# Performance work log

Measured on AMD Instinct MI355X. Metric: run time of the kernel, lower is better.

Reference implementation:

```python
import jax, jax.numpy as jnp
import numpy as np

N_NODES = 50000
N_EDGES = 500000
D_NODE = 256
D_EDGE = 256
FINAL_OUT = 256
NEG_SLOPE = 0.01  # torch LeakyReLU default


def _linear_params(key, d_in, d_out):
    kw, kb = jax.random.split(key)
    s = 1.0 / np.sqrt(d_in)
    W = jax.random.uniform(kw, (d_in, d_out), jnp.float32, -s, s)
    b = jax.random.uniform(kb, (d_out,), jnp.float32, -s, s)
    return W, b


def setup_inputs() -> dict:
    key = jax.random.key(0)
    ks = jax.random.split(key, 8)
    in1 = D_NODE + D_EDGE          # 512
    hid1 = 2 * in1                 # 1024
    out1 = hid1 // 2               # 512
    in2 = out1 + D_NODE            # 768
    hid2 = 2 * in2                 # 1536
    W1, b1 = _linear_params(ks[0], in1, hid1)
    W2, b2 = _linear_params(ks[1], hid1, out1)
    W3, b3 = _linear_params(ks[2], in2, hid2)
    W4, b4 = _linear_params(ks[3], hid2, FINAL_OUT)
    x = jax.random.normal(ks[4], (N_NODES, D_NODE), jnp.float32)
    edge_attr = jax.random.normal(ks[5], (N_EDGES, D_EDGE), jnp.float32)
    edge_index = jax.random.randint(ks[6], (2, N_EDGES), 0, N_NODES, jnp.int64)
    u = jax.random.normal(ks[7], (1, 16), jnp.float32)
    batch = jnp.zeros((N_NODES,), jnp.int64)
    return {"x": x, "edge_index": edge_index, "edge_attr": edge_attr,
            "u": u, "batch": batch,
            "W1": W1, "b1": b1, "W2": W2, "b2": b2,
            "W3": W3, "b3": b3, "W4": W4, "b4": b4}


def _leaky(v):
    return jnp.where(v >= 0, v, NEG_SLOPE * v)


def reference(x, edge_index, edge_attr, u, batch, W1, b1, W2, b2, W3, b3, W4, b4):
    row, col = edge_index[0], edge_index[1]
    # gather source-node features and concat edge features: [E, D_NODE+D_EDGE]
    m = jnp.concatenate([x[row], edge_attr], axis=1)
    # node_mlp_1
    m = _leaky(m @ W1 + b1) @ W2 + b2            # [E, out1]
    # scatter-mean over destination nodes (count clamped to 1, as torch_scatter)
    agg = jax.ops.segment_sum(m, col, num_segments=x.shape[0])
    cnt = jax.ops.segment_sum(jnp.ones((m.shape[0],), m.dtype), col,
                              num_segments=x.shape[0])
    agg = agg / jnp.maximum(cnt, 1.0)[:, None]   # [N, out1]
    # node_mlp_2
    h = jnp.concatenate([x, agg], axis=1)        # [N, in2]
    return _leaky(h @ W3 + b3) @ W4 + b4         # [N, FINAL_OUT]
```

## Files before the change

kernel.cpp:

```cpp
#include <hip/hip_runtime.h>

typedef __bf16 bf16x8 __attribute__((ext_vector_type(8)));
typedef float fx4 __attribute__((ext_vector_type(4)));
typedef unsigned short u16x8 __attribute__((ext_vector_type(8)));
typedef unsigned short u16x4 __attribute__((ext_vector_type(4)));

__device__ __forceinline__ unsigned short f2b(float f) {
  unsigned u = __float_as_uint(f);
  u = (u + 0x7fffu + ((u >> 16) & 1u)) >> 16;
  return (unsigned short)u;
}
__device__ __forceinline__ float b2f(unsigned short s) {
  return __uint_as_float((unsigned)s << 16);
}

__device__ __forceinline__ void gload16(const void* g, void* l) {
  __builtin_amdgcn_global_load_lds(
      (const __attribute__((address_space(1))) unsigned int*)g,
      (__attribute__((address_space(3))) unsigned int*)l, 16, 0, 0);
}

template<int MODE, int K, int N, int NT, bool EAB>
__global__ __launch_bounds__(256)
void gemm_k(const unsigned short* __restrict__ A,
            const unsigned short* __restrict__ xb,
            const unsigned short* __restrict__ eas,
            const float* __restrict__ eaf,
            const float* __restrict__ aggH_in,
            const float* __restrict__ cnt,
            const unsigned short* __restrict__ agg2b_in,
            const unsigned short* __restrict__ zxb,
            const int* __restrict__ perm,
            const int* __restrict__ ssrc,
            const int* __restrict__ sdst,
            const unsigned short* __restrict__ Bt,
            const float* __restrict__ bias,
            float* __restrict__ outf,
            unsigned short* __restrict__ outb,
            int M, int base, int mt, int mtc)
{
  const int bid = blockIdx.x;
  const int xcd = bid & 7;
  const int sl  = bid >> 3;
  const int tile_n = sl % NT;
  const int tile_m = xcd * mtc + sl / NT;
  if (tile_m >= mt) return;
  const int mbase = tile_m * 128;

  constexpr int SMEM = (MODE == 1) ? 51216 : ((MODE == 2) ? 16384 : 32768);
  __shared__ __align__(16) char smem[SMEM];

  const int t = threadIdx.x;
  const int w = t >> 6, l = t & 63;
  const int wr = w >> 1, wc = w & 1;
  const int lr = l & 15, lk = l >> 4;

  fx4 zero = {0.f, 0.f, 0.f, 0.f};
  fx4 acc[4][4];
#pragma unroll
  for (int i = 0; i < 4; i++)
#pragma unroll
    for (int j = 0; j < 4; j++) acc[i][j] = zero;

  auto STAGE = [&](int ks, int b) {
    const int k0 = ks * 32;
    char* Ab = (char*)smem + b * 16384;
    char* Bb = Ab + 8192;
#pragma unroll
    for (int it = 0; it < 2; ++it) {
      const int c = t + it * 256;
      const int row = c >> 2, u = c & 3;
      gload16(Bt + (size_t)(tile_n * 128 + row) * K + (k0 + u * 8),
              Bb + c * 16);
      int rl = mbase + row; if (rl >= M) rl = M - 1;
      if constexpr (MODE == 1) {
        if constexpr (EAB) {
          gload16(eas + (size_t)rl * 256 + (k0 + u * 8), Ab + c * 16);
        } else {
          const int e = perm[rl];
          const float* s = eaf + (size_t)e * 256 + (k0 + u * 8);
          fx4 f0 = *(const fx4*)s, f1 = *(const fx4*)(s + 4);
          u16x8 v;
          v[0]=f2b(f0[0]); v[1]=f2b(f0[1]); v[2]=f2b(f0[2]); v[3]=f2b(f0[3]);
          v[4]=f2b(f1[0]); v[5]=f2b(f1[1]); v[6]=f2b(f1[2]); v[7]=f2b(f1[3]);
          *(u16x8*)(Ab + c * 16) = v;
        }
      } else if constexpr (MODE == 2) {
        const float ct = cnt[rl];
        const float rs = 1.f / fmaxf(ct, 1.f);
        const float* s = aggH_in + (size_t)rl * 1024 + (k0 + u * 8);
        fx4 f0 = *(const fx4*)s, f1 = *(const fx4*)(s + 4);
        u16x8 v;
        v[0]=f2b(f0[0]*rs); v[1]=f2b(f0[1]*rs); v[2]=f2b(f0[2]*rs); v[3]=f2b(f0[3]*rs);
        v[4]=f2b(f1[0]*rs); v[5]=f2b(f1[1]*rs); v[6]=f2b(f1[2]*rs); v[7]=f2b(f1[3]*rs);
        *(u16x8*)(Ab + c * 16) = v;
      } else if constexpr (MODE == 3) {
        const int node = base + rl;
        if (k0 < 256)
          gload16(xb + (size_t)node * 256 + (k0 + u * 8), Ab + c * 16);
        else
          gload16(agg2b_in + (size_t)node * 512 + (k0 - 256) + u * 8,
                  Ab + c * 16);
      } else if constexpr (MODE == 5) {
        gload16(xb + (size_t)rl * 256 + (k0 + u * 8), Ab + c * 16);
      } else {
        gload16(A + (size_t)rl * K + (k0 + u * 8), Ab + c * 16);
      }
    }
  };

  auto COMPUTE = [&](int b) {
    const unsigned short* Al = (const unsigned short*)((char*)smem + b * 16384);
    const unsigned short* Bl = Al + 4096;
    bf16x8 af[4], bfr[4];
    const int mb0 = wr * 64, nb0 = wc * 64;
#pragma unroll
    for (int i = 0; i < 4; i++)
      af[i] = *(const bf16x8*)(Al + (mb0 + i * 16 + lr) * 32 + lk * 8);
#pragma unroll
    for (int j = 0; j < 4; j++)
      bfr[j] = *(const bf16x8*)(Bl + (nb0 + j * 16 + lr) * 32 + lk * 8);
#pragma unroll
    for (int i = 0; i < 4; i++)
#pragma unroll
      for (int j = 0; j < 4; j++)
        acc[i][j] = __builtin_amdgcn_mfma_f32_16x16x32_bf16(af[i], bfr[j],
                                                            acc[i][j], 0, 0, 0);
  };

  const int NK = K / 32;
  if constexpr (MODE == 1) {
#pragma unroll
    for (int q = 0; q < 8; ++q) {
      const int c = q * 256 + t;
      const int zrow = c >> 4, zu = c & 15;
      int gr = mbase + zrow; if (gr >= M) gr = M - 1;
      gload16(zxb + (size_t)ssrc[gr] * 1024 + tile_n * 128 + zu * 8,
              (char*)smem + 18448 + c * 16);
    }
    for (int ks = 0; ks < NK; ++ks) {
      STAGE(ks, 0);
      __syncthreads();
      COMPUTE(0);
      __syncthreads();
    }
  } else if constexpr (MODE == 2) {
    for (int ks = 0; ks < NK; ++ks) {
      STAGE(ks, 0);
      __syncthreads();
      COMPUTE(0);
      __syncthreads();
    }
  } else {
    STAGE(0, 0);
    for (int ks = 0; ks < NK; ++ks) {
      const int cur = ks & 1;
      if (ks + 1 < NK) {
        STAGE(ks + 1, cur ^ 1);
        asm volatile("s_waitcnt vmcnt(4)" ::: "memory");
      } else {
        asm volatile("s_waitcnt vmcnt(0)" ::: "memory");
      }
      __builtin_amdgcn_s_barrier();
      COMPUTE(cur);
      __builtin_amdgcn_s_barrier();
    }
  }

  if constexpr (MODE == 1) {
    int rows = M - mbase; if (rows > 128) rows = 128;
    unsigned short* CL = (unsigned short*)smem;
    int* runs_s = (int*)(smem + 16896);
    int* runs_e = (int*)(smem + 17408);
    int* runs_d = (int*)(smem + 17920);
    unsigned long long* wmask = (unsigned long long*)(smem + 18432);
    const unsigned short* ZL = (const unsigned short*)(smem + 18448);
    int flag = 0;
    if (t < 128)
      flag = (t < rows) && ((t == 0) || (sdst[mbase + t] != sdst[mbase + t - 1]));
    unsigned long long bm = __ballot(flag);
    if (l == 0 && w < 2) wmask[w] = bm;
    __syncthreads();
    const unsigned long long m0 = wmask[0], m1 = wmask[1];
    const int nruns = __builtin_popcountll(m0) + __builtin_popcountll(m1);
    if (flag) {
      int rank, rend;
      if (t < 64) {
        rank = __builtin_popcountll(m0 & ((t == 0) ? 0ull : ((1ull << t) - 1)));
        unsigned long long above = (t == 63) ? 0ull : (m0 & (~0ull << (t + 1)));
        if (above) rend = __builtin_ctzll(above);
        else if (m1) rend = 64 + __builtin_ctzll(m1);
        else rend = rows;
      } else {
        const int tt = t - 64;
        rank = __builtin_popcountll(m0) +
               __builtin_popcountll(m1 & ((tt == 0) ? 0ull : ((1ull << tt) - 1)));
        unsigned long long above = (tt == 63) ? 0ull : (m1 & (~0ull << (tt + 1)));
        rend = above ? 64 + __builtin_ctzll(above) : rows;
      }
      runs_s[rank] = t; runs_e[rank] = rend; runs_d[rank] = sdst[mbase + t];
    }
    const int lc = wc * 16 + lr;
    const int nn_base = tile_n * 128 + wc * 64 + lr;
    for (int jj = 0; jj < 2; ++jj) {
#pragma unroll
      for (int jp = 0; jp < 2; ++jp) {
        const int j = jj * 2 + jp;
        const float bj = bias[nn_base + j * 16];
        const int cloc = wc * 64 + j * 16 + lr;
#pragma unroll
        for (int i = 0; i < 4; i++)
#pragma unroll
          for (int r = 0; r < 4; r++) {
            const int lrow = wr * 64 + i * 16 + lk * 4 + r;
            float v = acc[i][j][r] + bj + b2f(ZL[lrow * 128 + cloc]);
            v = v >= 0.f ? v : 0.01f * v;
            CL[lrow * 66 + jp * 32 + lc] = f2b(v);
          }
      }
      __syncthreads();
      for (int task = t; task < nruns * 64; task += 256) {
        const int ri = task >> 6, c = task & 63;
        const int rs = runs_s[ri], re = runs_e[ri];
        float s = 0.f;
        for (int r = rs; r < re; ++r) s += b2f(CL[r * 66 + c]);
        const int jp = c >> 5, w16 = (c >> 4) & 1, clr = c & 15;
        const int n = tile_n * 128 + w16 * 64 + (jj * 2 + jp) * 16 + clr;
        float* addr = outf + (size_t)runs_d[ri] * 1024 + n;
        const bool open = (rs == 0 && mbase > 0) || (re == rows && mbase + rows < M);
        if (open) atomicAdd(addr, s); else *addr = s;
      }
      __syncthreads();
    }
  } else {
#pragma unroll
    for (int j = 0; j < 4; j++) {
      const int n = tile_n * 128 + wc * 64 + j * 16 + lr;
      float bj = 0.f;
      if constexpr (MODE == 2 || MODE == 3 || MODE == 4) bj = bias[n];
#pragma unroll
      for (int i = 0; i < 4; i++) {
        const int m0 = mbase + wr * 64 + i * 16 + lk * 4;
#pragma unroll
        for (int r = 0; r < 4; r++) {
          const int m = m0 + r;
          if (m < M) {
            float v = acc[i][j][r];
            if constexpr (MODE == 2) {
              v += (cnt[m] > 0.f ? bj : 0.f);
              outb[(size_t)m * N + n] = f2b(v);
            } else if constexpr (MODE == 3) {
              v += bj;
              v = v >= 0.f ? v : 0.01f * v;
              outb[(size_t)m * N + n] = f2b(v);
            } else if constexpr (MODE == 5) {
              outb[(size_t)m * N + n] = f2b(v);
            } else {
              outf[(size_t)(base + m) * N + n] = v + bj;
            }
          }
        }
      }
    }
  }
}

__global__ void fix_idx_k(const int* __restrict__ src, int* __restrict__ dst, int n2) {
  int i = blockIdx.x * blockDim.x + threadIdx.x;
  if (i >= n2) return;
  bool is64 = true;
#pragma unroll
  for (int p = 0; p < 16; ++p) is64 = is64 && (src[2 * p + 1] == 0);
  dst[i] = is64 ? src[2 * i] : src[i];
}

__global__ void cvt_f2b_k(const float* __restrict__ x, unsigned short* __restrict__ o,
                          long n4) {
  long i = (long)blockIdx.x * blockDim.x + threadIdx.x;
  if (i < n4) {
    fx4 f = *(const fx4*)(x + i * 4);
    u16x4 v; v[0]=f2b(f[0]); v[1]=f2b(f[1]); v[2]=f2b(f[2]); v[3]=f2b(f[3]);
    *(u16x4*)(o + i * 4) = v;
  }
}

__global__ void cvt_eas_k(const float* __restrict__ ea, const int* __restrict__ perm,
                          unsigned short* __restrict__ eas, int E) {
  long i = (long)blockIdx.x * blockDim.x + threadIdx.x;
  if (i >= (long)E * 64) return;
  const int s = (int)(i >> 6), q = (int)(i & 63);
  const float* src = ea + (size_t)perm[s] * 256 + q * 4;
  fx4 f = *(const fx4*)src;
  u16x4 v; v[0]=f2b(f[0]); v[1]=f2b(f[1]); v[2]=f2b(f[2]); v[3]=f2b(f[3]);
  *(u16x4*)(eas + (size_t)s * 256 + q * 4) = v;
}

__global__ void cvt_w_k(const float* __restrict__ W, unsigned short* __restrict__ Wt,
                        int K, int N) {
  long i = (long)blockIdx.x * blockDim.x + threadIdx.x;
  if (i < (long)K * N) {
    int k = (int)(i / N), n = (int)(i % N);
    Wt[(size_t)n * K + k] = f2b(W[i]);
  }
}

__global__ void cnt_kk(const int* __restrict__ ecol, float* __restrict__ cnt, int E) {
  int i = blockIdx.x * blockDim.x + threadIdx.x;
  if (i < E) atomicAdd(cnt + ecol[i], 1.f);
}

__global__ __launch_bounds__(1024)
void scan_k(const float* __restrict__ cnt, int* __restrict__ pos, int Nn) {
  __shared__ int sdata[1024];
  __shared__ int carry;
  if (threadIdx.x == 0) carry = 0;
  __syncthreads();
  for (int bb = 0; bb < Nn; bb += 1024) {
    const int i = bb + threadIdx.x;
    const int v = (i < Nn) ? (int)cnt[i] : 0;
    sdata[threadIdx.x] = v;
    __syncthreads();
    for (int off = 1; off < 1024; off <<= 1) {
      int tv = (threadIdx.x >= off) ? sdata[threadIdx.x - off] : 0;
      __syncthreads();
      sdata[threadIdx.x] += tv;
      __syncthreads();
    }
    const int excl = sdata[threadIdx.x] - v + carry;
    if (i < Nn) pos[i] = excl;
    __syncthreads();
    if (threadIdx.x == 1023) carry += sdata[1023];
    __syncthreads();
  }
}

__global__ void perm_k(const int* __restrict__ idx, int E, int* __restrict__ pos,
                       int* __restrict__ perm, int* __restrict__ ssrc,
                       int* __restrict__ sdst) {
  int e = blockIdx.x * blockDim.x + threadIdx.x;
  if (e >= E) return;
  const int d = idx[E + e];
  const int s = atomicAdd(pos + d, 1);
  perm[s] = e;
  ssrc[s] = idx[e];
  sdst[s] = d;
}

extern "C" void kernel_launch(void* const* d_in, const int* in_sizes, int n_in,
                              void* d_out, int out_size, void* d_ws, size_t ws_size,
                              hipStream_t stream)
{
  const float* x  = (const float*)d_in[0];
  const int* eraw = (const int*)d_in[1];
  const float* ea = (const float*)d_in[2];
  const float* W1 = (const float*)d_in[5];
  const float* b1 = (const float*)d_in[6];
  const float* W2 = (const float*)d_in[7];
  const float* b2 = (const float*)d_in[8];
  const float* W3 = (const float*)d_in[9];
  const float* b3 = (const float*)d_in[10];
  const float* W4 = (const float*)d_in[11];
  const float* b4 = (const float*)d_in[12];
  float* out = (float*)d_out;

  const int Nn = in_sizes[0] / 256;
  const int E  = in_sizes[1] / 2;

  char* p = (char*)d_ws;
  auto take = [&](size_t bytes) -> char* {
    char* r = p; p += (bytes + 255) & ~(size_t)255; return r;
  };
  unsigned short* W1xt = (unsigned short*)take((size_t)1024 * 256 * 2);
  unsigned short* W1et = (unsigned short*)take((size_t)1024 * 256 * 2);
  unsigned short* W2t  = (unsigned short*)take((size_t)1024 * 512 * 2);
  unsigned short* W3t  = (unsigned short*)take((size_t)768 * 1536 * 2);
  unsigned short* W4t  = (unsigned short*)take((size_t)1536 * 256 * 2);
  int* idx  = (int*)take((size_t)2 * E * 4);
  float* cnt  = (float*)take((size_t)Nn * 4);
  float* aggH = (float*)take((size_t)Nn * 1024 * 4);
  size_t zlen = (size_t)(p - (char*)cnt);
  unsigned short* agg2b = (unsigned short*)take((size_t)Nn * 512 * 2);
  unsigned short* xb    = (unsigned short*)take((size_t)Nn * 256 * 2);
  unsigned short* zxb   = (unsigned short*)take((size_t)Nn * 1024 * 2);
  int* pos  = (int*)take((size_t)Nn * 4);
  int* perm = (int*)take((size_t)E * 4);
  int* ssrc = (int*)take((size_t)E * 4);
  int* sdst = (int*)take((size_t)E * 4);

  long avail = (long)ws_size - (long)(p - (char*)d_ws);

  unsigned short* eas = nullptr;
  const long eas_bytes = (((long)E * 256 * 2) + 255) & ~255L;
  if (avail >= eas_bytes + 128 * 3072 + 1024) {
    eas = (unsigned short*)take((size_t)E * 256 * 2);
    avail -= eas_bytes;
  }
  long bandN = avail / 3072;  bandN &= ~127L;
  if (bandN > 50048) bandN = 50048;
  if (bandN < 128)   bandN = 128;
  unsigned short* H3 = (unsigned short*)take((size_t)bandN * 3072);

  hipMemsetAsync(cnt, 0, zlen, stream);
  fix_idx_k<<<(2 * E + 255) / 256, 256, 0, stream>>>(eraw, idx, 2 * E);
  cnt_kk<<<(E + 255) / 256, 256, 0, stream>>>(idx + E, cnt, E);
  scan_k<<<1, 1024, 0, stream>>>(cnt, pos, Nn);
  perm_k<<<(E + 255) / 256, 256, 0, stream>>>(idx, E, pos, perm, ssrc, sdst);
  cvt_f2b_k<<<(Nn * 64 + 255) / 256, 256, 0, stream>>>(x, xb, (long)Nn * 64);
  if (eas)
    cvt_eas_k<<<(int)(((long)E * 64 + 255) / 256), 256, 0, stream>>>(ea, perm,
                                                                     eas, E);
  cvt_w_k<<<(256 * 1024 + 255) / 256, 256, 0, stream>>>(W1, W1xt, 256, 1024);
  cvt_w_k<<<(256 * 1024 + 255) / 256, 256, 0, stream>>>(W1 + 256 * 1024, W1et,
                                                        256, 1024);
  cvt_w_k<<<(1024 * 512 + 255) / 256, 256, 0, stream>>>(W2, W2t, 1024, 512);
  cvt_w_k<<<(768 * 1536 + 255) / 256, 256, 0, stream>>>(W3, W3t, 768, 1536);
  cvt_w_k<<<(1536 * 256 + 255) / 256, 256, 0, stream>>>(W4, W4t, 1536, 256);

  {
    const int mt = (Nn + 127) / 128, mtc = (mt + 7) / 8;
    gemm_k<5, 256, 1024, 8, false><<<mtc * 8 * 8, 256, 0, stream>>>(
        nullptr, xb, nullptr, nullptr, nullptr, nullptr, nullptr, nullptr,
        nullptr, nullptr, nullptr, W1xt, nullptr, nullptr, zxb, Nn, 0, mt, mtc);
  }

  {
    const int mt = (E + 127) / 128, mtc = (mt + 7) / 8;
    const int grid = mtc * 8 * 8;
    if (eas)
      gemm_k<1, 256, 1024, 8, true><<<grid, 256, 0, stream>>>(
          nullptr, nullptr, eas, ea, nullptr, nullptr, nullptr, zxb, perm,
          ssrc, sdst, W1et, b1, aggH, nullptr, E, 0, mt, mtc);
    else
      gemm_k<1, 256, 1024, 8, false><<<grid, 256, 0, stream>>>(
          nullptr, nullptr, nullptr, ea, nullptr, nullptr, nullptr, zxb, perm,
          ssrc, sdst, W1et, b1, aggH, nullptr, E, 0, mt, mtc);
  }

  {
    const int mt = (Nn + 127) / 128, mtc = (mt + 7) / 8;
    gemm_k<2, 1024, 512, 4, false><<<mtc * 8 * 4, 256, 0, stream>>>(
        nullptr, nullptr, nullptr, nullptr, aggH, cnt, nullptr, nullptr,
        nullptr, nullptr, nullptr, W2t, b2, nullptr, agg2b, Nn, 0, mt, mtc);
  }

  for (long base = 0; base < Nn; base += bandN) {
    long rem = Nn - base;
    int mb = (int)(rem < bandN ? rem : bandN);
    int mt = (mb + 127) / 128, mtc = (mt + 7) / 8;
    gemm_k<3, 768, 1536, 12, false><<<mtc * 8 * 12, 256, 0, stream>>>(
        nullptr, xb, nullptr, nullptr, nullptr, nullptr, agg2b, nullptr,
        nullptr, nullptr, nullptr, W3t, b3, nullptr, H3, mb, (int)base, mt, mtc);
    gemm_k<4, 1536, 256, 2, false><<<mtc * 8 * 2, 256, 0, stream>>>(
        H3, nullptr, nullptr, nullptr, nullptr, nullptr, nullptr, nullptr,
        nullptr, nullptr, nullptr, W4t, b4, out, nullptr, mb, (int)base, mt, mtc);
  }
}
```

Baseline: 1.629 ms.

## Halve gathered-Z LDS buffer in edge GEMM and replace full aggH memset with targeted zeroing

The edge MLP GEMM epilogue now stages the gathered node-projection tile in two 64-column halves, loading the second half after the first half's epilogue. This cuts LDS from about 51KB to about 35KB, and the launch bounds now request 4 blocks per CU so more waves can be resident. The full memset of the 200MB aggH buffer is replaced by two small kernels. One zeroes only the destination rows that sit on tile boundaries and are accumulated with atomics; the other zeroes rows of nodes with no incoming edges. This relies on every other row being written by a plain store, and the second Z gather adds latency in the middle of the epilogue.

```diff
diff --git a/kernel.cpp b/kernel.cpp
--- a/kernel.cpp
+++ b/kernel.cpp
@@ -21,7 +21,7 @@
 }
 
 template<int MODE, int K, int N, int NT, bool EAB>
-__global__ __launch_bounds__(256)
+__global__ __launch_bounds__(256, (MODE == 1) ? 4 : 1)
 void gemm_k(const unsigned short* __restrict__ A,
             const unsigned short* __restrict__ xb,
             const unsigned short* __restrict__ eas,
@@ -47,7 +47,7 @@
   if (tile_m >= mt) return;
   const int mbase = tile_m * 128;
 
-  constexpr int SMEM = (MODE == 1) ? 51216 : ((MODE == 2) ? 16384 : 32768);
+  constexpr int SMEM = (MODE == 1) ? 34832 : ((MODE == 2) ? 16384 : 32768);
   __shared__ __align__(16) char smem[SMEM];
 
   const int t = threadIdx.x;
@@ -128,16 +128,20 @@
                                                             acc[i][j], 0, 0, 0);
   };
 
+  auto ZSTAGE = [&](int h) {
+#pragma unroll
+    for (int q2 = 0; q2 < 4; ++q2) {
+      const int c = q2 * 256 + t;
+      const int zrow = c >> 3, u = c & 7;
+      int gr = mbase + zrow; if (gr >= M) gr = M - 1;
+      const int coff = tile_n * 128 + ((u & 4) ? 64 : 0) + h * 32 + (u & 3) * 8;
+      gload16(zxb + (size_t)ssrc[gr] * 1024 + coff, (char*)smem + 16896 + c * 16);
+    }
+  };
+
   const int NK = K / 32;
   if constexpr (MODE == 1) {
-#pragma unroll
-    for (int q = 0; q < 8; ++q) {
-      const int c = q * 256 + t;
-      const int zrow = c >> 4, zu = c & 15;
-      int gr = mbase + zrow; if (gr >= M) gr = M - 1;
-      gload16(zxb + (size_t)ssrc[gr] * 1024 + tile_n * 128 + zu * 8,
-              (char*)smem + 18448 + c * 16);
-    }
+    ZSTAGE(0);
     for (int ks = 0; ks < NK; ++ks) {
       STAGE(ks, 0);
       __syncthreads();
@@ -170,11 +174,11 @@
   if constexpr (MODE == 1) {
     int rows = M - mbase; if (rows > 128) rows = 128;
     unsigned short* CL = (unsigned short*)smem;
-    int* runs_s = (int*)(smem + 16896);
-    int* runs_e = (int*)(smem + 17408);
-    int* runs_d = (int*)(smem + 17920);
-    unsigned long long* wmask = (unsigned long long*)(smem + 18432);
-    const unsigned short* ZL = (const unsigned short*)(smem + 18448);
+    unsigned short* ZLh = (unsigned short*)(smem + 16896);
+    int* runs_s = (int*)(smem + 33280);
+    int* runs_e = (int*)(smem + 33792);
+    int* runs_d = (int*)(smem + 34304);
+    unsigned long long* wmask = (unsigned long long*)(smem + 34816);
     int flag = 0;
     if (t < 128)
       flag = (t < rows) && ((t == 0) || (sdst[mbase + t] != sdst[mbase + t - 1]));
@@ -207,18 +211,19 @@
       for (int jp = 0; jp < 2; ++jp) {
         const int j = jj * 2 + jp;
         const float bj = bias[nn_base + j * 16];
-        const int cloc = wc * 64 + j * 16 + lr;
+        const int q = wc * 32 + jp * 16 + lr;
 #pragma unroll
         for (int i = 0; i < 4; i++)
 #pragma unroll
           for (int r = 0; r < 4; r++) {
             const int lrow = wr * 64 + i * 16 + lk * 4 + r;
-            float v = acc[i][j][r] + bj + b2f(ZL[lrow * 128 + cloc]);
+            float v = acc[i][j][r] + bj + b2f(ZLh[lrow * 64 + q]);
             v = v >= 0.f ? v : 0.01f * v;
             CL[lrow * 66 + jp * 32 + lc] = f2b(v);
           }
       }
       __syncthreads();
+      if (jj == 0) ZSTAGE(1);
       for (int task = t; task < nruns * 64; task += 256) {
         const int ri = task >> 6, c = task & 63;
         const int rs = runs_s[ri], re = runs_e[ri];
@@ -309,6 +314,24 @@
   if (i < E) atomicAdd(cnt + ecol[i], 1.f);
 }
 
+__global__ void zb_k(const int* __restrict__ sdst, float* __restrict__ aggH,
+                     int M, int mt) {
+  const int b = blockIdx.x;
+  int row = (b >> 1) * 128 + ((b & 1) ? 127 : 0);
+  if (row >= M) row = M - 1;
+  const int dest = sdst[row];
+  fx4 z = {0.f, 0.f, 0.f, 0.f};
+  *(fx4*)(aggH + (size_t)dest * 1024 + threadIdx.x * 4) = z;
+}
+
+__global__ void zc_k(const float* __restrict__ cnt, float* __restrict__ aggH,
+                     int Nn) {
+  const int nidx = blockIdx.x;
+  if (nidx >= Nn || cnt[nidx] != 0.f) return;
+  fx4 z = {0.f, 0.f, 0.f, 0.f};
+  *(fx4*)(aggH + (size_t)nidx * 1024 + threadIdx.x * 4) = z;
+}
+
 __global__ __launch_bounds__(1024)
 void scan_k(const float* __restrict__ cnt, int* __restrict__ pos, int Nn) {
   __shared__ int sdata[1024];
@@ -378,7 +401,6 @@
   int* idx  = (int*)take((size_t)2 * E * 4);
   float* cnt  = (float*)take((size_t)Nn * 4);
   float* aggH = (float*)take((size_t)Nn * 1024 * 4);
-  size_t zlen = (size_t)(p - (char*)cnt);
   unsigned short* agg2b = (unsigned short*)take((size_t)Nn * 512 * 2);
   unsigned short* xb    = (unsigned short*)take((size_t)Nn * 256 * 2);
   unsigned short* zxb   = (unsigned short*)take((size_t)Nn * 1024 * 2);
@@ -400,11 +422,15 @@
   if (bandN < 128)   bandN = 128;
   unsigned short* H3 = (unsigned short*)take((size_t)bandN * 3072);
 
-  hipMemsetAsync(cnt, 0, zlen, stream);
+  const int mtE = (E + 127) / 128;
+
+  hipMemsetAsync(cnt, 0, (size_t)Nn * 4, stream);
   fix_idx_k<<<(2 * E + 255) / 256, 256, 0, stream>>>(eraw, idx, 2 * E);
   cnt_kk<<<(E + 255) / 256, 256, 0, stream>>>(idx + E, cnt, E);
   scan_k<<<1, 1024, 0, stream>>>(cnt, pos, Nn);
   perm_k<<<(E + 255) / 256, 256, 0, stream>>>(idx, E, pos, perm, ssrc, sdst);
+  zb_k<<<mtE * 2, 256, 0, stream>>>(sdst, aggH, E, mtE);
+  zc_k<<<Nn, 256, 0, stream>>>(cnt, aggH, Nn);
   cvt_f2b_k<<<(Nn * 64 + 255) / 256, 256, 0, stream>>>(x, xb, (long)Nn * 64);
   if (eas)
     cvt_eas_k<<<(int)(((long)E * 64 + 255) / 256), 256, 0, stream>>>(ea, perm,
@@ -424,7 +450,7 @@
   }
 
   {
-    const int mt = (E + 127) / 128, mtc = (mt + 7) / 8;
+    const int mt = mtE, mtc = (mt + 7) / 8;
     const int grid = mtc * 8 * 8;
     if (eas)
       gemm_k<1, 256, 1024, 8, true><<<grid, 256, 0, stream>>>(
```

New measurement: 1.573 ms. 3.5% less time.
